# Optimization experiments

Measured on AMD Instinct MI355X. Metric: run time of the kernel, lower is better.

The kernel has to match this reference:

```python
import jax, jax.numpy as jnp
import numpy as np

NEG_INF = -1000000000.0
B, S, E, H = 2, 2048, 1024, 16
HD = E // H


def setup_inputs() -> dict:
    key = jax.random.key(0)
    ks = jax.random.split(key, 5)
    sd = 1.0 / np.sqrt(E)
    return {
        "x": jax.random.normal(ks[0], (B, S, E), dtype=jnp.float32),
        "Wqkv": jax.random.normal(ks[1], (3 * E, E), dtype=jnp.float32) * sd,
        "bqkv": jax.random.normal(ks[2], (3 * E,), dtype=jnp.float32) * sd,
        "Wout": jax.random.normal(ks[3], (E, E), dtype=jnp.float32) * sd,
        "bout": jax.random.normal(ks[4], (E,), dtype=jnp.float32) * sd,
    }


def reference(x, Wqkv, bqkv, Wout, bout):
    # qkv projection (torch Linear: x @ W.T + b)
    qkv = x @ Wqkv.T + bqkv                      # [B, S, 3E]
    qkv = qkv.reshape(B, S, H, 3 * HD).transpose(0, 2, 1, 3)  # [B, H, S, 3*hd]
    q, k, v = jnp.split(qkv, 3, axis=-1)          # each [B, H, S, hd]
    scaled = jnp.einsum('bhqd,bhkd->bhqk', q, k) / jnp.sqrt(jnp.float32(HD))
    # faithful to source: mask = tril(ones) * NEG_INF (lower triangle incl. diagonal gets -1e9)
    mask = jnp.tril(jnp.ones((S, S), dtype=jnp.float32)) * NEG_INF
    scaled = scaled + mask                        # broadcast over [B, H]
    attention = jax.nn.softmax(scaled, axis=-1)
    values = jnp.einsum('bhqk,bhkd->bhqd', attention, v)
    values = values.transpose(0, 2, 1, 3).reshape(B, S, E)
    out = values @ Wout.T + bout
    return out
```

## Files before the change

### kernel.cpp

```cpp
#include <hip/hip_runtime.h>
#include <hip/hip_bf16.h>
#include <math.h>

#define Bb 2
#define Ss 2048
#define Ee 1024
#define Hh 16
#define HDd 64
#define NEG_INF_F -1000000000.0f

typedef __attribute__((ext_vector_type(8))) short bfrag;
typedef __attribute__((ext_vector_type(4))) float ffrag;
typedef __attribute__((ext_vector_type(16))) float ffrag16;
typedef __attribute__((ext_vector_type(8))) unsigned short us8;

#define C1F 0.1803368801f

#define WAIT_VM6 0x0F76
#define WAIT_VM4 0x0F74
#define WAIT_VM0 0x0F70

__device__ __forceinline__ unsigned short f2bf(float x) {
  unsigned u = __float_as_uint(x);
  u += 0x7fffu + ((u >> 16) & 1u);
  return (unsigned short)(u >> 16);
}
__device__ __forceinline__ float bf2f(unsigned short h) {
  return __uint_as_float(((unsigned)h) << 16);
}

__device__ __forceinline__ void async_copy16(void* lds, const void* g) {
  __builtin_amdgcn_global_load_lds(
      (const __attribute__((address_space(1))) unsigned int*)g,
      (__attribute__((address_space(3))) unsigned int*)lds, 16, 0, 0);
}

__global__ __launch_bounds__(256) void split_all(
    const float* __restrict__ x, unsigned short* __restrict__ xh,
    const float* __restrict__ wq, unsigned short* __restrict__ wqh,
    unsigned short* __restrict__ wql,
    const float* __restrict__ wo, unsigned short* __restrict__ woh,
    unsigned short* __restrict__ wol) {
  int bid = blockIdx.x;
  const float* in;
  unsigned short *hi, *lo;
  if (bid < 4096) { in = x; hi = xh; lo = nullptr; }
  else if (bid < 7168) { bid -= 4096; in = wq; hi = wqh; lo = wql; }
  else { bid -= 7168; in = wo; hi = woh; lo = wol; }
  const int idx = (bid * 256 + threadIdx.x) * 4;
  const float4 v = *(const float4*)(in + idx);
  unsigned short h0 = f2bf(v.x), h1 = f2bf(v.y), h2 = f2bf(v.z), h3 = f2bf(v.w);
  ushort4 hv = {h0, h1, h2, h3};
  *(ushort4*)(hi + idx) = hv;
  if (lo) {
    ushort4 lv = {f2bf(v.x - bf2f(h0)), f2bf(v.y - bf2f(h1)),
                  f2bf(v.z - bf2f(h2)), f2bf(v.w - bf2f(h3))};
    *(ushort4*)(lo + idx) = lv;
  }
}

__device__ __forceinline__ int gemm_slot(int row, int q) {
  return (row >> 1) * 8 + ((((row & 1) * 4) | q) ^ ((row >> 1) & 7));
}
__device__ __forceinline__ int slot_src_off(int slot, int ld) {
  const int dr = slot >> 3;
  const int idx8 = (slot & 7) ^ (dr & 7);
  const int row = dr * 2 + (idx8 >> 2);
  const int q = idx8 & 3;
  return row * ld + q * 8;
}

__global__ __launch_bounds__(256) void gemm_qkv(
    const unsigned short* __restrict__ Ah,
    const unsigned short* __restrict__ Bh, const unsigned short* __restrict__ Bl,
    const float* __restrict__ bias,
    unsigned short* __restrict__ q_h, unsigned short* __restrict__ k_h,
    unsigned short* __restrict__ vt_h) {
  __shared__ unsigned short sm[3 * 12288];
  const int tid = threadIdx.x;
  const int lane = tid & 63;
  const int w = tid >> 6;
  const int wm = w >> 1;
  const int wn = w & 1;
  const int l31 = lane & 31;
  const int e = lane >> 5;
  const int m0 = blockIdx.x * 128;
  const int n0 = blockIdx.y * 128;

  int coff[2], ldsb[2];
#pragma unroll
  for (int u = 0; u < 2; ++u) {
    const int slot = w * 128 + u * 64 + lane;
    coff[u] = slot_src_off(slot, 1024);
    ldsb[u] = (w * 128 + u * 64) * 8;
  }
  const unsigned short* srcs[3] = {
      Ah + (size_t)m0 * 1024, Bh + (size_t)n0 * 1024, Bl + (size_t)n0 * 1024};

  ffrag16 acc[2][2];
#pragma unroll
  for (int i = 0; i < 2; ++i)
#pragma unroll
    for (int j = 0; j < 2; ++j) acc[i][j] = (ffrag16)0.f;

  int ca[2][2], cb[2][2];
#pragma unroll
  for (int t = 0; t < 2; ++t)
#pragma unroll
    for (int h2 = 0; h2 < 2; ++h2) {
      ca[t][h2] = gemm_slot(wm * 64 + t * 32 + l31, h2 * 2 + e) * 8;
      cb[t][h2] = gemm_slot(wn * 64 + t * 32 + l31, h2 * 2 + e) * 8;
    }

#pragma unroll
  for (int t = 0; t < 3; ++t)
#pragma unroll
    for (int u = 0; u < 2; ++u)
      async_copy16(&sm[0 + t * 4096 + ldsb[u]], srcs[t] + coff[u] + 0);
#pragma unroll
  for (int t = 0; t < 3; ++t)
#pragma unroll
    for (int u = 0; u < 2; ++u)
      async_copy16(&sm[12288 + t * 4096 + ldsb[u]], srcs[t] + coff[u] + 32);

  int b0 = 0, b1 = 12288, b2 = 24576;
  for (int k = 0; k < 32; ++k) {
    if (k < 31) __builtin_amdgcn_s_waitcnt(WAIT_VM6);
    else        __builtin_amdgcn_s_waitcnt(WAIT_VM0);
    __builtin_amdgcn_s_barrier();
    __builtin_amdgcn_sched_barrier(0);
    if (k + 2 < 32) {
      const int k0 = (k + 2) * 32;
#pragma unroll
      for (int t = 0; t < 3; ++t)
#pragma unroll
        for (int u = 0; u < 2; ++u)
          async_copy16(&sm[b2 + t * 4096 + ldsb[u]], srcs[t] + coff[u] + k0);
    }

    bfrag ah[2][2], bhf[2][2], blf[2][2];
#pragma unroll
    for (int t = 0; t < 2; ++t)
#pragma unroll
      for (int h2 = 0; h2 < 2; ++h2) {
        ah[t][h2] = *(const bfrag*)&sm[b0 + 0 + ca[t][h2]];
        bhf[t][h2] = *(const bfrag*)&sm[b0 + 4096 + cb[t][h2]];
        blf[t][h2] = *(const bfrag*)&sm[b0 + 8192 + cb[t][h2]];
      }
#pragma unroll
    for (int mt = 0; mt < 2; ++mt)
#pragma unroll
      for (int nt = 0; nt < 2; ++nt)
#pragma unroll
        for (int h2 = 0; h2 < 2; ++h2) {
          acc[mt][nt] = __builtin_amdgcn_mfma_f32_32x32x16_bf16(
              ah[mt][h2], bhf[nt][h2], acc[mt][nt], 0, 0, 0);
          acc[mt][nt] = __builtin_amdgcn_mfma_f32_32x32x16_bf16(
              ah[mt][h2], blf[nt][h2], acc[mt][nt], 0, 0, 0);
        }
    const int tb = b0; b0 = b1; b1 = b2; b2 = tb;
  }

#pragma unroll
  for (int nt = 0; nt < 2; ++nt) {
    const int n = n0 + wn * 64 + nt * 32 + l31;
    const float bv = bias[n];
    const int h = n / 192;
    const int c = n - h * 192;
    const int d = c & 63;
#pragma unroll
    for (int mt = 0; mt < 2; ++mt) {
      if (c >= 128) {
#pragma unroll
        for (int g = 0; g < 4; ++g) {
          const int m = m0 + wm * 64 + mt * 32 + g * 8 + e * 4;
          const int bidx = m >> 11;
          const int s = m & 2047;
          ushort4 hv4;
          unsigned short* ph = (unsigned short*)&hv4;
#pragma unroll
          for (int r = 0; r < 4; ++r)
            ph[r] = f2bf(acc[mt][nt][g * 4 + r] + bv);
          const size_t off =
              (size_t)(bidx * 16 + h) * (64 * 2048) + (size_t)d * 2048 + s;
          *(ushort4*)(vt_h + off) = hv4;
        }
      } else {
        const float scale = (c < 64) ? C1F : 1.0f;
        unsigned short* dh = (c < 64) ? q_h : k_h;
#pragma unroll
        for (int g = 0; g < 4; ++g)
#pragma unroll
          for (int r = 0; r < 4; ++r) {
            const int m = m0 + wm * 64 + mt * 32 + g * 8 + e * 4 + r;
            const int bidx = m >> 11;
            const int s = m & 2047;
            const size_t off =
                (size_t)(bidx * 16 + h) * (2048 * 64) + (size_t)s * 64 + d;
            dh[off] = f2bf((acc[mt][nt][g * 4 + r] + bv) * scale);
          }
      }
    }
  }
}

__global__ __launch_bounds__(256) void gemm_out2(
    const unsigned short* __restrict__ A,
    const unsigned short* __restrict__ Bh, const unsigned short* __restrict__ Bl,
    const float* __restrict__ bias, float* __restrict__ out) {
  __shared__ unsigned short sm[3 * 8192];
  const int tid = threadIdx.x;
  const int lane = tid & 63;
  const int w = tid >> 6;
  const int wm = w >> 1;
  const int wn = w & 1;
  const int l31 = lane & 31;
  const int e = lane >> 5;
  const int m0 = blockIdx.x * 128;
  const int n0 = blockIdx.y * 64;

  int acoff[2], aldsb[2];
#pragma unroll
  for (int u = 0; u < 2; ++u) {
    const int slot = w * 128 + u * 64 + lane;
    acoff[u] = slot_src_off(slot, 1024);
    aldsb[u] = (w * 128 + u * 64) * 8;
  }
  const int bslot = w * 64 + lane;
  const int bcoff = slot_src_off(bslot, 1024);
  const int bldsb = bslot * 8;

  const unsigned short* Ap  = A + (size_t)m0 * 1024;
  const unsigned short* Bph = Bh + (size_t)n0 * 1024;
  const unsigned short* Bpl = Bl + (size_t)n0 * 1024;

  ffrag16 acc[2];
  acc[0] = (ffrag16)0.f;
  acc[1] = (ffrag16)0.f;

  int ca[2][2], cb[2];
#pragma unroll
  for (int t = 0; t < 2; ++t)
#pragma unroll
    for (int h2 = 0; h2 < 2; ++h2)
      ca[t][h2] = gemm_slot(wm * 64 + t * 32 + l31, h2 * 2 + e) * 8;
#pragma unroll
  for (int h2 = 0; h2 < 2; ++h2)
    cb[h2] = gemm_slot(wn * 32 + l31, h2 * 2 + e) * 8;

  {
#pragma unroll
    for (int u = 0; u < 2; ++u)
      async_copy16(&sm[0 + aldsb[u]], Ap + acoff[u] + 0);
    async_copy16(&sm[0 + 4096 + bldsb], Bph + bcoff + 0);
    async_copy16(&sm[0 + 6144 + bldsb], Bpl + bcoff + 0);
#pragma unroll
    for (int u = 0; u < 2; ++u)
      async_copy16(&sm[8192 + aldsb[u]], Ap + acoff[u] + 32);
    async_copy16(&sm[8192 + 4096 + bldsb], Bph + bcoff + 32);
    async_copy16(&sm[8192 + 6144 + bldsb], Bpl + bcoff + 32);
  }

  int b0 = 0, b1 = 8192, b2 = 16384;
  for (int k = 0; k < 32; ++k) {
    if (k < 31) __builtin_amdgcn_s_waitcnt(WAIT_VM4);
    else        __builtin_amdgcn_s_waitcnt(WAIT_VM0);
    __builtin_amdgcn_s_barrier();
    __builtin_amdgcn_sched_barrier(0);
    if (k + 2 < 32) {
      const int k0 = (k + 2) * 32;
#pragma unroll
      for (int u = 0; u < 2; ++u)
        async_copy16(&sm[b2 + aldsb[u]], Ap + acoff[u] + k0);
      async_copy16(&sm[b2 + 4096 + bldsb], Bph + bcoff + k0);
      async_copy16(&sm[b2 + 6144 + bldsb], Bpl + bcoff + k0);
    }

    bfrag ah[2][2], bhf[2], blf[2];
#pragma unroll
    for (int t = 0; t < 2; ++t)
#pragma unroll
      for (int h2 = 0; h2 < 2; ++h2)
        ah[t][h2] = *(const bfrag*)&sm[b0 + ca[t][h2]];
#pragma unroll
    for (int h2 = 0; h2 < 2; ++h2) {
      bhf[h2] = *(const bfrag*)&sm[b0 + 4096 + cb[h2]];
      blf[h2] = *(const bfrag*)&sm[b0 + 6144 + cb[h2]];
    }
#pragma unroll
    for (int mt = 0; mt < 2; ++mt)
#pragma unroll
      for (int h2 = 0; h2 < 2; ++h2) {
        acc[mt] = __builtin_amdgcn_mfma_f32_32x32x16_bf16(
            ah[mt][h2], bhf[h2], acc[mt], 0, 0, 0);
        acc[mt] = __builtin_amdgcn_mfma_f32_32x32x16_bf16(
            ah[mt][h2], blf[h2], acc[mt], 0, 0, 0);
      }
    const int tb = b0; b0 = b1; b1 = b2; b2 = tb;
  }

  const int n = n0 + wn * 32 + l31;
  const float bv = bias[n];
#pragma unroll
  for (int mt = 0; mt < 2; ++mt)
#pragma unroll
    for (int g = 0; g < 4; ++g)
#pragma unroll
      for (int r = 0; r < 4; ++r) {
        const int m = m0 + wm * 64 + mt * 32 + g * 8 + e * 4 + r;
        out[(size_t)m * 1024 + n] = acc[mt][g * 4 + r] + bv;
      }
}

__global__ __launch_bounds__(256, 4) void attn_2ph(
    const unsigned short* __restrict__ qh, const unsigned short* __restrict__ kh,
    const unsigned short* __restrict__ vth, unsigned short* __restrict__ vals) {
  __shared__ unsigned short sm[2 * 8192 + 4096];
  const int tid = threadIdx.x;
  const int lane = tid & 63;
  const int w = tid >> 6;
  const int l15 = lane & 15;
  const int quad = lane >> 4;
  const int bh = blockIdx.x;
  const int y = blockIdx.y;
  const size_t base = (size_t)bh * (Ss * HDd);
  const int b = bh >> 4;
  const int h = bh & 15;
  const int PB = 16384;

  const int c0 = w * 128 + lane;
  const int c1 = c0 + 64;
  const int r0 = c0 >> 3, r1 = c1 >> 3;
  const int s0 = ((c0 & 7) ^ (r0 & 7)) * 8;
  const int s1 = ((c1 & 7) ^ (r1 & 7)) * 8;
  const int koff0 = r0 * 64 + s0, koff1 = r1 * 64 + s1;
  const int voff0 = r0 * 2048 + s0, voff1 = r1 * 2048 + s1;
  const int ldsc0 = c0 * 8;
  const int ldsc1 = c1 * 8;

  bfrag vone;
#pragma unroll
  for (int j = 0; j < 8; ++j) vone[j] = (short)0x3F80;

  const bool fixw = (y == 0) && (w == 3);
  ffrag Vsum[4];
#pragma unroll
  for (int dt = 0; dt < 4; ++dt) Vsum[dt] = (ffrag)0.f;

  for (int ph = 0; ph < 2; ++ph) {
    const int ybk = ph ? (31 - y) : y;
    const int rb = 64 * ybk + 16 * w;

    bfrag Qf[2];
#pragma unroll
    for (int ks = 0; ks < 2; ++ks)
      Qf[ks] = *(const bfrag*)(qh + base + (size_t)(rb + l15) * 64 + ks * 32 + quad * 8);

    ffrag O[4], Oe;
#pragma unroll
    for (int dt = 0; dt < 4; ++dt) O[dt] = (ffrag)0.f;
    Oe = (ffrag)0.f;

    int cur = 0, nxt = 8192;
    {
      const unsigned short* kp = kh + base + ybk * 4096;
      const unsigned short* vp = vth + base + ybk * 64;
      async_copy16(&sm[cur + ldsc0], kp + koff0);
      async_copy16(&sm[cur + ldsc1], kp + koff1);
      async_copy16(&sm[cur + 4096 + ldsc0], vp + voff0);
      async_copy16(&sm[cur + 4096 + ldsc1], vp + voff1);
    }

    for (int kt = ybk; kt < 32; ++kt) {
      __syncthreads();
      if (kt + 1 < 32) {
        const unsigned short* kp = kh + base + (kt + 1) * 4096;
        const unsigned short* vp = vth + base + (kt + 1) * 64;
        async_copy16(&sm[nxt + ldsc0], kp + koff0);
        async_copy16(&sm[nxt + ldsc1], kp + koff1);
        async_copy16(&sm[nxt + 4096 + ldsc0], vp + voff0);
        async_copy16(&sm[nxt + 4096 + ldsc1], vp + voff1);
      }

      ffrag S[4];
#pragma unroll
      for (int nt = 0; nt < 4; ++nt) S[nt] = (ffrag)0.f;
#pragma unroll
      for (int nt = 0; nt < 4; ++nt) {
        const int krow = nt * 16 + l15;
#pragma unroll
        for (int ks = 0; ks < 2; ++ks) {
          const bfrag kbh =
              *(const bfrag*)&sm[cur + krow * 64 + ((ks * 4 + quad) ^ (krow & 7)) * 8];
          S[nt] = __builtin_amdgcn_mfma_f32_16x16x32_bf16(Qf[ks], kbh, S[nt], 0, 0, 0);
        }
      }

      const float CM = -1.442695041e9f;
      const bool partial = (kt == ybk);
#pragma unroll
      for (int nt = 0; nt < 4; ++nt) {
        const int key = nt * 16 + l15;
#pragma unroll
        for (int rp = 0; rp < 2; ++rp) {
          float t0 = S[nt][2 * rp];
          float t1 = S[nt][2 * rp + 1];
          if (partial) {
            const int jg = kt * 64 + key;
            const int ig = rb + quad * 4 + 2 * rp;
            if (jg <= ig) t0 += CM;
            if (jg <= ig + 1) t1 += CM;
          }
          float2 pf;
          pf.x = __builtin_amdgcn_exp2f(t0);
          pf.y = __builtin_amdgcn_exp2f(t1);
          const __hip_bfloat162 pb = __float22bfloat162_rn(pf);
          const unsigned short* pbs = (const unsigned short*)&pb;
          const int pr0 = w * 16 + quad * 4 + 2 * rp;
          sm[PB + pr0 * 64 + (((key >> 3) ^ (pr0 & 7)) * 8 + (key & 7))] = pbs[0];
          const int pr1 = pr0 + 1;
          sm[PB + pr1 * 64 + (((key >> 3) ^ (pr1 & 7)) * 8 + (key & 7))] = pbs[1];
        }
      }

#pragma unroll
      for (int ks = 0; ks < 2; ++ks) {
        const int prow = w * 16 + l15;
        const bfrag pA =
            *(const bfrag*)&sm[PB + prow * 64 + ((ks * 4 + quad) ^ (prow & 7)) * 8];
        Oe = __builtin_amdgcn_mfma_f32_16x16x32_bf16(pA, vone, Oe, 0, 0, 0);
#pragma unroll
        for (int dt = 0; dt < 4; ++dt) {
          const int vrow = dt * 16 + l15;
          const bfrag vbh =
              *(const bfrag*)&sm[cur + 4096 + vrow * 64 + ((ks * 4 + quad) ^ (vrow & 7)) * 8];
          O[dt] = __builtin_amdgcn_mfma_f32_16x16x32_bf16(pA, vbh, O[dt], 0, 0, 0);
          if (fixw && ph == 0)
            Vsum[dt] = __builtin_amdgcn_mfma_f32_16x16x32_bf16(vone, vbh, Vsum[dt], 0, 0, 0);
        }
      }
      const int t = cur; cur = nxt; nxt = t;
    }

#pragma unroll
    for (int r = 0; r < 4; ++r) {
      const float inv = 1.0f / Oe[r];
      const int s = rb + quad * 4 + r;
      const size_t rowoff = ((size_t)b * 2048 + s) * 1024 + h * 64;
#pragma unroll
      for (int dt = 0; dt < 4; ++dt) {
        float val = O[dt][r] * inv;
        if (fixw && ph == 1 && quad == 3 && r == 3)
          val = Vsum[dt][3] * (1.0f / 2048.0f);
        vals[rowoff + dt * 16 + l15] = f2bf(val);
      }
    }
    __syncthreads();
  }
}

extern "C" void kernel_launch(void* const* d_in, const int* in_sizes, int n_in,
                              void* d_out, int out_size, void* d_ws, size_t ws_size,
                              hipStream_t stream) {
  const float* x    = (const float*)d_in[0];
  const float* Wqkv = (const float*)d_in[1];
  const float* bqkv = (const float*)d_in[2];
  const float* Wout = (const float*)d_in[3];
  const float* bout = (const float*)d_in[4];
  float* out = (float*)d_out;
  char* wsb = (char*)d_ws;

  unsigned short* qhp  = (unsigned short*)d_ws;
  unsigned short* khp  = qhp + 1 * 4194304;
  unsigned short* vthp = qhp + 2 * 4194304;
  unsigned short* vals = qhp + 3 * 4194304;
  unsigned short* wqh  = (unsigned short*)(wsb + (48u << 20));
  unsigned short* wql  = (unsigned short*)(wsb + (54u << 20));
  unsigned short* woh  = (unsigned short*)(wsb + (60u << 20));
  unsigned short* wol  = (unsigned short*)(wsb + (62u << 20));
  unsigned short* xh   = (unsigned short*)d_out;

  dim3 blk(256);
  split_all<<<8192, blk, 0, stream>>>(x, xh, Wqkv, wqh, wql, Wout, woh, wol);
  gemm_qkv<<<dim3(32, 24), blk, 0, stream>>>(xh, wqh, wql, bqkv, qhp, khp, vthp);
  attn_2ph<<<dim3(32, 16), blk, 0, stream>>>(qhp, khp, vthp, vals);
  gemm_out2<<<dim3(32, 16), blk, 0, stream>>>(vals, woh, wol, bout, out);
}
```

Measured before the change: 204.3 us.

## Switch projection GEMMs from triple to double LDS buffering with priority-boosted MFMA

Both projection GEMMs now use two LDS stages instead of three. Each iteration issues the next tile's async loads, waits for the current tile, reads LDS fragments, then places a second barrier before the MFMA block. The MFMA block runs under raised wave priority. Smaller LDS use may let more blocks fit per CU. The cost is one less stage of prefetch distance and an extra barrier per k-step.

```diff
diff --git a/kernel.cpp b/kernel.cpp
--- a/kernel.cpp
+++ b/kernel.cpp
@@ -16,9 +16,10 @@
 
 #define C1F 0.1803368801f
 
-#define WAIT_VM6 0x0F76
-#define WAIT_VM4 0x0F74
-#define WAIT_VM0 0x0F70
+#define WAIT_VM6   0x0F76
+#define WAIT_VM4   0x0F74
+#define WAIT_VM0   0x0F70
+#define WAIT_LGKM0 0xC07F
 
 __device__ __forceinline__ unsigned short f2bf(float x) {
   unsigned u = __float_as_uint(x);
@@ -76,7 +77,7 @@
     const float* __restrict__ bias,
     unsigned short* __restrict__ q_h, unsigned short* __restrict__ k_h,
     unsigned short* __restrict__ vt_h) {
-  __shared__ unsigned short sm[3 * 12288];
+  __shared__ unsigned short sm[2 * 12288];
   const int tid = threadIdx.x;
   const int lane = tid & 63;
   const int w = tid >> 6;
@@ -117,36 +118,37 @@
 #pragma unroll
     for (int u = 0; u < 2; ++u)
       async_copy16(&sm[0 + t * 4096 + ldsb[u]], srcs[t] + coff[u] + 0);
-#pragma unroll
-  for (int t = 0; t < 3; ++t)
-#pragma unroll
-    for (int u = 0; u < 2; ++u)
-      async_copy16(&sm[12288 + t * 4096 + ldsb[u]], srcs[t] + coff[u] + 32);
-
-  int b0 = 0, b1 = 12288, b2 = 24576;
+
+  int cur = 0, nxt = 12288;
   for (int k = 0; k < 32; ++k) {
-    if (k < 31) __builtin_amdgcn_s_waitcnt(WAIT_VM6);
-    else        __builtin_amdgcn_s_waitcnt(WAIT_VM0);
+    if (k + 1 < 32) {
+      const int k0 = (k + 1) * 32;
+#pragma unroll
+      for (int t = 0; t < 3; ++t)
+#pragma unroll
+        for (int u = 0; u < 2; ++u)
+          async_copy16(&sm[nxt + t * 4096 + ldsb[u]], srcs[t] + coff[u] + k0);
+      __builtin_amdgcn_s_waitcnt(WAIT_VM6);
+    } else {
+      __builtin_amdgcn_s_waitcnt(WAIT_VM0);
+    }
     __builtin_amdgcn_s_barrier();
     __builtin_amdgcn_sched_barrier(0);
-    if (k + 2 < 32) {
-      const int k0 = (k + 2) * 32;
-#pragma unroll
-      for (int t = 0; t < 3; ++t)
-#pragma unroll
-        for (int u = 0; u < 2; ++u)
-          async_copy16(&sm[b2 + t * 4096 + ldsb[u]], srcs[t] + coff[u] + k0);
-    }
 
     bfrag ah[2][2], bhf[2][2], blf[2][2];
 #pragma unroll
     for (int t = 0; t < 2; ++t)
 #pragma unroll
       for (int h2 = 0; h2 < 2; ++h2) {
-        ah[t][h2] = *(const bfrag*)&sm[b0 + 0 + ca[t][h2]];
-        bhf[t][h2] = *(const bfrag*)&sm[b0 + 4096 + cb[t][h2]];
-        blf[t][h2] = *(const bfrag*)&sm[b0 + 8192 + cb[t][h2]];
-      }
+        ah[t][h2] = *(const bfrag*)&sm[cur + 0 + ca[t][h2]];
+        bhf[t][h2] = *(const bfrag*)&sm[cur + 4096 + cb[t][h2]];
+        blf[t][h2] = *(const bfrag*)&sm[cur + 8192 + cb[t][h2]];
+      }
+    __builtin_amdgcn_s_waitcnt(WAIT_LGKM0);
+    __builtin_amdgcn_sched_barrier(0);
+    __builtin_amdgcn_s_barrier();
+
+    __builtin_amdgcn_s_setprio(1);
 #pragma unroll
     for (int mt = 0; mt < 2; ++mt)
 #pragma unroll
@@ -158,7 +160,8 @@
           acc[mt][nt] = __builtin_amdgcn_mfma_f32_32x32x16_bf16(
               ah[mt][h2], blf[nt][h2], acc[mt][nt], 0, 0, 0);
         }
-    const int tb = b0; b0 = b1; b1 = b2; b2 = tb;
+    __builtin_amdgcn_s_setprio(0);
+    const int tb = cur; cur = nxt; nxt = tb;
   }
 
 #pragma unroll
@@ -208,7 +211,7 @@
     const unsigned short* __restrict__ A,
     const unsigned short* __restrict__ Bh, const unsigned short* __restrict__ Bl,
     const float* __restrict__ bias, float* __restrict__ out) {
-  __shared__ unsigned short sm[3 * 8192];
+  __shared__ unsigned short sm[2 * 8192];
   const int tid = threadIdx.x;
   const int lane = tid & 63;
   const int w = tid >> 6;
@@ -254,39 +257,40 @@
       async_copy16(&sm[0 + aldsb[u]], Ap + acoff[u] + 0);
     async_copy16(&sm[0 + 4096 + bldsb], Bph + bcoff + 0);
     async_copy16(&sm[0 + 6144 + bldsb], Bpl + bcoff + 0);
-#pragma unroll
-    for (int u = 0; u < 2; ++u)
-      async_copy16(&sm[8192 + aldsb[u]], Ap + acoff[u] + 32);
-    async_copy16(&sm[8192 + 4096 + bldsb], Bph + bcoff + 32);
-    async_copy16(&sm[8192 + 6144 + bldsb], Bpl + bcoff + 32);
-  }
-
-  int b0 = 0, b1 = 8192, b2 = 16384;
+  }
+
+  int cur = 0, nxt = 8192;
   for (int k = 0; k < 32; ++k) {
-    if (k < 31) __builtin_amdgcn_s_waitcnt(WAIT_VM4);
-    else        __builtin_amdgcn_s_waitcnt(WAIT_VM0);
+    if (k + 1 < 32) {
+      const int k0 = (k + 1) * 32;
+#pragma unroll
+      for (int u = 0; u < 2; ++u)
+        async_copy16(&sm[nxt + aldsb[u]], Ap + acoff[u] + k0);
+      async_copy16(&sm[nxt + 4096 + bldsb], Bph + bcoff + k0);
+      async_copy16(&sm[nxt + 6144 + bldsb], Bpl + bcoff + k0);
+      __builtin_amdgcn_s_waitcnt(WAIT_VM4);
+    } else {
+      __builtin_amdgcn_s_waitcnt(WAIT_VM0);
+    }
     __builtin_amdgcn_s_barrier();
     __builtin_amdgcn_sched_barrier(0);
-    if (k + 2 < 32) {
-      const int k0 = (k + 2) * 32;
-#pragma unroll
-      for (int u = 0; u < 2; ++u)
-        async_copy16(&sm[b2 + aldsb[u]], Ap + acoff[u] + k0);
-      async_copy16(&sm[b2 + 4096 + bldsb], Bph + bcoff + k0);
-      async_copy16(&sm[b2 + 6144 + bldsb], Bpl + bcoff + k0);
-    }
 
     bfrag ah[2][2], bhf[2], blf[2];
 #pragma unroll
     for (int t = 0; t < 2; ++t)
 #pragma unroll
       for (int h2 = 0; h2 < 2; ++h2)
-        ah[t][h2] = *(const bfrag*)&sm[b0 + ca[t][h2]];
+        ah[t][h2] = *(const bfrag*)&sm[cur + ca[t][h2]];
 #pragma unroll
     for (int h2 = 0; h2 < 2; ++h2) {
-      bhf[h2] = *(const bfrag*)&sm[b0 + 4096 + cb[h2]];
-      blf[h2] = *(const bfrag*)&sm[b0 + 6144 + cb[h2]];
-    }
+      bhf[h2] = *(const bfrag*)&sm[cur + 4096 + cb[h2]];
+      blf[h2] = *(const bfrag*)&sm[cur + 6144 + cb[h2]];
+    }
+    __builtin_amdgcn_s_waitcnt(WAIT_LGKM0);
+    __builtin_amdgcn_sched_barrier(0);
+    __builtin_amdgcn_s_barrier();
+
+    __builtin_amdgcn_s_setprio(1);
 #pragma unroll
     for (int mt = 0; mt < 2; ++mt)
 #pragma unroll
@@ -296,7 +300,8 @@
         acc[mt] = __builtin_amdgcn_mfma_f32_32x32x16_bf16(
             ah[mt][h2], blf[h2], acc[mt], 0, 0, 0);
       }
-    const int tb = b0; b0 = b1; b1 = b2; b2 = tb;
+    __builtin_amdgcn_s_setprio(0);
+    const int tb = cur; cur = nxt; nxt = tb;
   }
 
   const int n = n0 + wn * 32 + l31;
```

Result: no change. 204.1 us (-0.1%).
